# Kernel optimization log

Measured on AMD Instinct MI355X. Metric: run time of the kernel, lower is better.

## Reference

```python
import jax, jax.numpy as jnp
import numpy as np

H = 1024   # longformer-large hidden size
D = 256    # transformer d_model / args.hidden_dim
Q = 100    # num_queries / num_slots
N = 1024   # document length (unpadded tokens)
L = 30     # args.max_span_length
WD = 20    # span width embedding dim
S = N * L - L * (L - 1) // 2  # 30285 candidate spans


def _ln(x, g, b, eps=1e-5):
    m = jnp.mean(x, -1, keepdims=True)
    v = jnp.mean((x - m) ** 2, -1, keepdims=True)
    return (x - m) * jax.lax.rsqrt(v + eps) * g + b


def setup_inputs():
    ks = jax.random.split(jax.random.key(0), 16)
    # deterministic span enumeration: triu(0) & tril(L-1) mention mask, row-major
    idx = np.arange(N)
    m = (idx[None, :] >= idx[:, None]) & (idx[None, :] < idx[:, None] + L)
    ss, ee = np.nonzero(m)
    assert ss.shape[0] == S
    r = lambda i, shape, s=0.02: jax.random.normal(ks[i], shape, jnp.float32) * s
    z = lambda *shape: jnp.zeros(shape, jnp.float32)
    o = lambda *shape: jnp.ones(shape, jnp.float32)
    return dict(
        encoded_doc=jax.random.normal(ks[0], (1, N, H), jnp.float32),
        span_starts=jnp.asarray(ss, jnp.int32),
        span_ends=jnp.asarray(ee, jnp.int32),
        w_word_attn=r(1, (H, 1)), b_word_attn=z(1),
        span_width_embed=r(2, (L, WD)),
        w_span_proj=r(3, (3 * H + WD, D)), b_span_proj=z(D),
        slots_query=r(4, (Q, D)),
        wq=r(5, (D, D)), bq=z(D),
        wk=r(6, (D, D)), bk=z(D),
        wv=r(7, (D, D)), bv=z(D),
        w_ih=r(8, (3 * D, D)), w_hh=r(9, (3 * D, D)), b_ih=z(3 * D), b_hh=z(3 * D),
        w_mlp1=r(10, (D, 2 * D)), b_mlp1=z(2 * D),
        w_mlp2=r(11, (2 * D, D)), b_mlp2=z(D),
        g_in=o(D), beta_in=z(D),
        g_sl=o(D), beta_sl=z(D),
        g_ff=o(D), beta_ff=z(D),
    )


def reference(encoded_doc, span_starts, span_ends, w_word_attn, b_word_attn,
              span_width_embed, w_span_proj, b_span_proj, slots_query,
              wq, bq, wk, bk, wv, bv, w_ih, w_hh, b_ih, b_hh,
              w_mlp1, b_mlp1, w_mlp2, b_mlp2,
              g_in, beta_in, g_sl, beta_sl, g_ff, beta_ff):
    doc = encoded_doc[0]                                   # [N, H]
    # --- get_span_emb ---
    start_emb = doc[span_starts]                           # [S, H]
    end_emb = doc[span_ends]                               # [S, H]
    width_idx = jnp.minimum(1 + span_ends - span_starts, L) - 1
    width_emb = span_width_embed[width_idx]                # [S, WD]
    word_attn = (doc @ w_word_attn)[:, 0] + b_word_attn[0] # [N]
    pos = jnp.arange(N)
    smask = (pos[None, :] >= span_starts[:, None]) & (pos[None, :] <= span_ends[:, None])
    scores = jnp.where(smask, word_attn[None, :], -jnp.inf)  # log(mask)+attn
    head = jax.nn.softmax(scores, axis=-1) @ doc           # [S, H]
    span_emb = jnp.concatenate([start_emb, end_emb, width_emb, head], -1)[None]  # [1,S,3H+WD]
    x = span_emb @ w_span_proj + b_span_proj               # [1, S, D]
    # --- slot attention ---
    inputs = _ln(x, g_in, beta_in)
    k = inputs @ wk + bk
    v = inputs @ wv + bv
    scale = D ** -0.5
    eps = 1e-8
    slots = slots_query[None]                              # [1, Q, D]
    for _ in range(3):
        slots_prev = slots
        q = _ln(slots, g_sl, beta_sl) @ wq + bq
        dots = jnp.einsum('bid,bjd->bij', q, k) * scale    # [1, Q, S]
        attn = jax.nn.softmax(dots, axis=1) + eps          # softmax over slots!
        attn = attn / jnp.sum(attn, -1, keepdims=True)
        updates = jnp.einsum('bjd,bij->bid', v, attn)      # [1, Q, D]
        # torch GRUCell
        xg = updates.reshape(-1, D)
        h = slots_prev.reshape(-1, D)
        gi = xg @ w_ih.T + b_ih
        gh = h @ w_hh.T + b_hh
        ir, iz, inn = jnp.split(gi, 3, -1)
        hr, hz, hn = jnp.split(gh, 3, -1)
        rg = jax.nn.sigmoid(ir + hr)
        zg = jax.nn.sigmoid(iz + hz)
        ng = jnp.tanh(inn + rg * hn)
        slots = ((1.0 - zg) * ng + zg * h).reshape(1, -1, D)
        ff = _ln(slots, g_ff, beta_ff)
        slots = slots + jax.nn.relu(ff @ w_mlp1 + b_mlp1) @ w_mlp2 + b_mlp2
    q = _ln(slots, g_sl, beta_sl) @ wq + bq
    dots = jnp.einsum('bid,bjd->bij', q, k) * scale
    coref_logits = jnp.minimum(jax.nn.softmax(dots, axis=1) + eps, 1.0)  # [1, Q, S]
    return coref_logits, inputs
```

## Files before the change

kernel.cpp:

```cpp
#include <hip/hip_runtime.h>

#define S_TOT 30285
#define SPAD  30720
#define EPS_S 3.0285e-4f

typedef __attribute__((ext_vector_type(8))) short bf16x8;
typedef __attribute__((ext_vector_type(4))) float f32x4;

__device__ __forceinline__ unsigned short f2bf(float f) {
  unsigned u = __float_as_uint(f);
  u += 0x7FFFu + ((u >> 16) & 1u);
  return (unsigned short)(u >> 16);
}
__device__ __forceinline__ float allred_sum(float v) {
#pragma unroll
  for (int o = 32; o > 0; o >>= 1) v += __shfl_xor(v, o, 64);
  return v;
}


__global__ void k_word_attn(const float* __restrict__ doc, const float* __restrict__ w,
                            const float* __restrict__ b, float* __restrict__ wa) {
  int n = blockIdx.x, t = threadIdx.x;
  float s = 0.f;
  for (int h = t; h < 1024; h += 256) s += doc[n * 1024 + h] * w[h];
  __shared__ float red[256];
  red[t] = s;
  __syncthreads();
  for (int o = 128; o; o >>= 1) {
    if (t < o) red[t] += red[t + o];
    __syncthreads();
  }
  if (t == 0) wa[n] = red[0] + b[0];
}

__global__ void k_wd(const float* __restrict__ wemb, const float* __restrict__ wp,
                     float* __restrict__ wd) {
  int w = blockIdx.x, d = threadIdx.x;
  float s = 0.f;
  for (int j = 0; j < 20; j++) s += wemb[w * 20 + j] * wp[(2048 + j) * 256 + d];
  wd[w * 256 + d] = s;
}

__global__ void k_cast3(const float* __restrict__ doc, const float* __restrict__ wih,
                        const float* __restrict__ whh, unsigned short* __restrict__ docb,
                        unsigned short* __restrict__ wihb, unsigned short* __restrict__ whhb) {
  int b = blockIdx.x, t = threadIdx.x;
  if (b < 4096) {
    int i = b * 256 + t;
    docb[i] = f2bf(doc[i]);
  } else if (b < 4864) {
    int i = (b - 4096) * 256 + t;
    wihb[i] = f2bf(wih[i]);
  } else {
    int i = (b - 4864) * 256 + t;
    whhb[i] = f2bf(whh[i]);
  }
}

__global__ void k_tcast_all(const float* __restrict__ wsp, const float* __restrict__ wk,
                            const float* __restrict__ wv, const float* __restrict__ wq,
                            const float* __restrict__ w1, const float* __restrict__ w2,
                            unsigned short* __restrict__ wspT, unsigned short* __restrict__ wkT,
                            unsigned short* __restrict__ wvT, unsigned short* __restrict__ wqT,
                            unsigned short* __restrict__ w1T, unsigned short* __restrict__ w2T) {
  int b = blockIdx.x, t = threadIdx.x;
  const float* src;
  unsigned short* dst;
  int R, C, tid;
  if (b < 768) {
    int sec = b >> 8;
    tid = b & 255;
    src = wsp + (sec == 0 ? 0 : (sec == 1 ? 1024 * 256 : 2068 * 256));
    dst = wspT + (size_t)sec * 256 * 1024;
    R = 1024; C = 256;
  } else if (b < 832) { src = wk; dst = wkT; R = 256; C = 256; tid = b - 768; }
  else if (b < 896) { src = wv; dst = wvT; R = 256; C = 256; tid = b - 832; }
  else if (b < 960) { src = wq; dst = wqT; R = 256; C = 256; tid = b - 896; }
  else if (b < 1088) { src = w1; dst = w1T; R = 256; C = 512; tid = b - 960; }
  else { src = w2; dst = w2T; R = 512; C = 256; tid = b - 1088; }
  int cw = C >> 5;
  int c0 = (tid % cw) * 32, r0 = (tid / cw) * 32;
  __shared__ float tile[32][33];
#pragma unroll
  for (int i = 0; i < 4; i++) {
    int e = i * 256 + t, rr = e >> 5, cc = e & 31;
    tile[rr][cc] = src[(size_t)(r0 + rr) * C + c0 + cc];
  }
  __syncthreads();
#pragma unroll
  for (int i = 0; i < 4; i++) {
    int e = i * 256 + t, cc = e >> 5, rr = e & 31;
    dst[(size_t)(c0 + cc) * R + r0 + rr] = f2bf(tile[rr][cc]);
  }
}

__global__ __launch_bounds__(256) void k_abc_mfma(const unsigned short* __restrict__ docb,
                                                  const unsigned short* __restrict__ wspT,
                                                  float* __restrict__ A, float* __restrict__ B,
                                                  float* __restrict__ C) {
  int rt = blockIdx.x, sec = blockIdx.y;
  float* out = sec == 0 ? A : (sec == 1 ? B : C);
  const unsigned short* wt = wspT + (size_t)sec * 256 * 1024;
  __shared__ unsigned short lds[64 * 256];
  int t = threadIdx.x, w = t >> 6, l = t & 63, lr = l & 15, lh = l >> 4;
  f32x4 acc[4][4];
#pragma unroll
  for (int m = 0; m < 4; m++)
#pragma unroll
    for (int n = 0; n < 4; n++) acc[m][n] = (f32x4){0.f, 0.f, 0.f, 0.f};
  for (int kt = 0; kt < 4; kt++) {
    __syncthreads();
#pragma unroll
    for (int it = 0; it < 8; it++) {
      int e = it * 256 + t, row = e >> 5, c16 = e & 31;
      int ba = ((row * 512) + c16 * 16) ^ ((row & 7) << 4);
      *(uint4*)((char*)lds + ba) =
          *(const uint4*)(docb + (size_t)(rt * 64 + row) * 1024 + kt * 256 + c16 * 8);
    }
    __syncthreads();
    for (int kk = 0; kk < 8; kk++) {
      bf16x8 afr[4];
#pragma unroll
      for (int m = 0; m < 4; m++) {
        int row = m * 16 + lr;
        int ba = ((row * 512) + kk * 64 + lh * 16) ^ ((row & 7) << 4);
        afr[m] = *(bf16x8*)((char*)lds + ba);
      }
#pragma unroll
      for (int n = 0; n < 4; n++) {
        bf16x8 b8 = *(const bf16x8*)(wt + (size_t)(w * 64 + n * 16 + lr) * 1024 + kt * 256 +
                                     kk * 32 + lh * 8);
#pragma unroll
        for (int m = 0; m < 4; m++)
          acc[m][n] = __builtin_amdgcn_mfma_f32_16x16x32_bf16(afr[m], b8, acc[m][n], 0, 0, 0);
      }
    }
  }
#pragma unroll
  for (int n = 0; n < 4; n++) {
    int col = w * 64 + n * 16 + lr;
#pragma unroll
    for (int m = 0; m < 4; m++)
#pragma unroll
      for (int r = 0; r < 4; r++)
        out[(size_t)(rt * 64 + m * 16 + lh * 4 + r) * 256 + col] = acc[m][n][r];
  }
}

__global__ void k_spans_ln(const float* __restrict__ wa, const float* __restrict__ A,
                           const float* __restrict__ B, const float* __restrict__ C,
                           const float* __restrict__ Wd, const float* __restrict__ bias,
                           const float* __restrict__ g_in, const float* __restrict__ be_in,
                           float* __restrict__ xin, unsigned short* __restrict__ inb) {
  int ss = blockIdx.x, t = threadIdx.x;
  int wave = t >> 6, lane = t & 63;
  int nsp = min(30, 1024 - ss);
  int base = (ss < 995) ? ss * 30 : 29850 + 435 - ((1024 - ss) * (1025 - ss)) / 2;
  __shared__ float C_l[30 * 256];
  __shared__ float wa_l[30];
  __shared__ float red[8];
  for (int e = t; e < nsp * 256; e += 256)
    C_l[e] = C[(ss + (e >> 8)) * 256 + (e & 255)];
  if (t < nsp) wa_l[t] = wa[ss + t];
  __syncthreads();
  float aS = A[ss * 256 + t] + bias[t];
  float gg = g_in[t], bb = be_in[t];
  float m = -3.4e38f, Z = 0.f, W = 0.f;
  for (int sp = 0; sp < nsp; sp++) {
    float as_ = wa_l[sp];
    float mn = fmaxf(m, as_);
    float corr = __expf(m - mn);
    float e = __expf(as_ - mn);
    Z = Z * corr + e;
    W = W * corr + e * C_l[sp * 256 + t];
    m = mn;
    float val = aS + B[(ss + sp) * 256 + t] + Wd[sp * 256 + t] + W / Z;
    float s = allred_sum(val);
    if (lane == 0) red[wave] = s;
    __syncthreads();
    float mean = (red[0] + red[1] + red[2] + red[3]) * (1.f / 256.f);
    float dv = val - mean;
    float s2 = allred_sum(dv * dv);
    if (lane == 0) red[4 + wave] = s2;
    __syncthreads();
    float var = (red[4] + red[5] + red[6] + red[7]) * (1.f / 256.f);
    float o = dv * rsqrtf(var + 1e-5f) * gg + bb;
    size_t r = (size_t)(base + sp) * 256 + t;
    xin[r] = o;
    inb[r] = f2bf(o);
    __syncthreads();
  }
}

__global__ __launch_bounds__(256) void k_kv_mfma(const unsigned short* __restrict__ inb,
                                                 const unsigned short* __restrict__ wkT,
                                                 const unsigned short* __restrict__ wvT,
                                                 const float* __restrict__ bk,
                                                 const float* __restrict__ bv,
                                                 unsigned short* __restrict__ kb,
                                                 unsigned short* __restrict__ vT,
                                                 float* __restrict__ vsum) {
  int j0 = blockIdx.x * 64;
  int t = threadIdx.x, w = t >> 6, l = t & 63, lr = l & 15, lh = l >> 4;
  __shared__ unsigned short lds[64 * 256];
#pragma unroll
  for (int it = 0; it < 8; it++) {
    int e = it * 256 + t, row = e >> 5, c16 = e & 31;
    int ba = ((row * 512) + c16 * 16) ^ ((row & 7) << 4);
    *(uint4*)((char*)lds + ba) = *(const uint4*)(inb + (size_t)(j0 + row) * 256 + c16 * 8);
  }
  __syncthreads();
  f32x4 ak[4][4], av[4][4];
#pragma unroll
  for (int m = 0; m < 4; m++)
#pragma unroll
    for (int n = 0; n < 4; n++) {
      ak[m][n] = (f32x4){0.f, 0.f, 0.f, 0.f};
      av[m][n] = (f32x4){0.f, 0.f, 0.f, 0.f};
    }
  for (int kk = 0; kk < 8; kk++) {
    bf16x8 afr[4];
#pragma unroll
    for (int m = 0; m < 4; m++) {
      int row = m * 16 + lr;
      int ba = ((row * 512) + kk * 64 + lh * 16) ^ ((row & 7) << 4);
      afr[m] = *(bf16x8*)((char*)lds + ba);
    }
#pragma unroll
    for (int n = 0; n < 4; n++) {
      int col = w * 64 + n * 16 + lr;
      bf16x8 bk8 = *(const bf16x8*)(wkT + (size_t)col * 256 + kk * 32 + lh * 8);
      bf16x8 bv8 = *(const bf16x8*)(wvT + (size_t)col * 256 + kk * 32 + lh * 8);
#pragma unroll
      for (int m = 0; m < 4; m++) {
        ak[m][n] = __builtin_amdgcn_mfma_f32_16x16x32_bf16(afr[m], bk8, ak[m][n], 0, 0, 0);
        av[m][n] = __builtin_amdgcn_mfma_f32_16x16x32_bf16(afr[m], bv8, av[m][n], 0, 0, 0);
      }
    }
  }
#pragma unroll
  for (int n = 0; n < 4; n++) {
    int col = w * 64 + n * 16 + lr;
    float bks = bk[col], bvs = bv[col];
    float cs = 0.f;
#pragma unroll
    for (int m = 0; m < 4; m++)
#pragma unroll
      for (int r = 0; r < 4; r++) {
        int row = j0 + m * 16 + lh * 4 + r;
        float kvv = ak[m][n][r] + bks;
        float vvv = av[m][n][r] + bvs;
        kb[(size_t)row * 256 + col] = f2bf(kvv);
        vT[(size_t)col * SPAD + row] = f2bf(vvv);
        if (row < S_TOT) cs += vvv;
      }
    cs += __shfl_xor(cs, 16, 64);
    cs += __shfl_xor(cs, 32, 64);
    if (lh == 0) atomicAdd(&vsum[col], cs);
  }
}

__global__ void k_lnq(const float* __restrict__ src, float* __restrict__ slots_w,
                      unsigned short* __restrict__ lnslb, unsigned short* __restrict__ hbf,
                      const float* __restrict__ g, const float* __restrict__ be, int do_copy) {
  int i = blockIdx.x, t = threadIdx.x;
  if (i >= 100) {
    lnslb[i * 256 + t] = 0;
    hbf[i * 256 + t] = 0;
    return;
  }
  int wave = t >> 6, lane = t & 63;
  __shared__ float red[8];
  float v = src[i * 256 + t];
  if (do_copy) slots_w[i * 256 + t] = v;
  hbf[i * 256 + t] = f2bf(v);
  float s = allred_sum(v);
  if (lane == 0) red[wave] = s;
  __syncthreads();
  float mean = (red[0] + red[1] + red[2] + red[3]) * (1.f / 256.f);
  float dv = v - mean;
  float s2 = allred_sum(dv * dv);
  if (lane == 0) red[4 + wave] = s2;
  __syncthreads();
  float var = (red[4] + red[5] + red[6] + red[7]) * (1.f / 256.f);
  float rstd = rsqrtf(var + 1e-5f);
  lnslb[i * 256 + t] = f2bf(dv * rstd * g[t] + be[t]);
}

__global__ __launch_bounds__(256) void k_qmm(const unsigned short* __restrict__ lnslb,
                                             const unsigned short* __restrict__ wqT,
                                             const float* __restrict__ bq,
                                             unsigned short* __restrict__ qbf,
                                             float* __restrict__ rowsum) {
  int t = threadIdx.x;
  if (blockIdx.x == 0 && t < 128) rowsum[t] = 0.f;
  int w = t >> 6, l = t & 63, lr = l & 15, lh = l >> 4;
  int col = blockIdx.x * 64 + w * 16 + lr;
  f32x4 acc[7];
#pragma unroll
  for (int m = 0; m < 7; m++) acc[m] = (f32x4){0.f, 0.f, 0.f, 0.f};
  for (int kk = 0; kk < 8; kk++) {
    int d0 = kk * 32 + lh * 8;
    bf16x8 b8 = *(const bf16x8*)(wqT + (size_t)col * 256 + d0);
#pragma unroll
    for (int m = 0; m < 7; m++) {
      bf16x8 a8 = *(const bf16x8*)(lnslb + (size_t)(m * 16 + lr) * 256 + d0);
      acc[m] = __builtin_amdgcn_mfma_f32_16x16x32_bf16(a8, b8, acc[m], 0, 0, 0);
    }
  }
  float bb = bq[col];
#pragma unroll
  for (int m = 0; m < 7; m++)
#pragma unroll
    for (int r = 0; r < 4; r++)
      qbf[(size_t)(m * 16 + lh * 4 + r) * 256 + col] = f2bf(acc[m][r] + bb);
}

__global__ __launch_bounds__(256) void k_dots_f(const unsigned short* __restrict__ kb,
                                                const unsigned short* __restrict__ qb,
                                                unsigned short* __restrict__ pT,
                                                float* __restrict__ rowsum,
                                                float* __restrict__ uraw,
                                                float* __restrict__ coref, int final_, int S_) {
  int j0 = blockIdx.x * 64;
  int t = threadIdx.x, w = t >> 6, l = t & 63, lr = l & 15, lh = l >> 4;
  if (!final_ && blockIdx.x == 0) {
    for (int e = t; e < 112 * 256; e += 256) uraw[e] = 0.f;
  }
  f32x4 acc[7];
#pragma unroll
  for (int n = 0; n < 7; n++) acc[n] = (f32x4){0.f, 0.f, 0.f, 0.f};
  const unsigned short* arow = kb + (size_t)(j0 + w * 16 + lr) * 256;
  for (int kk = 0; kk < 8; kk++) {
    bf16x8 a8 = *(const bf16x8*)(arow + kk * 32 + lh * 8);
#pragma unroll
    for (int n = 0; n < 7; n++) {
      bf16x8 b8 = *(const bf16x8*)(qb + (size_t)(n * 16 + lr) * 256 + kk * 32 + lh * 8);
      acc[n] = __builtin_amdgcn_mfma_f32_16x16x32_bf16(a8, b8, acc[n], 0, 0, 0);
    }
  }
  __shared__ float dt[64][117];
#pragma unroll
  for (int n = 0; n < 7; n++)
#pragma unroll
    for (int r = 0; r < 4; r++) dt[w * 16 + lh * 4 + r][n * 16 + lr] = acc[n][r] * 0.0625f;
  __syncthreads();
  int jj = t >> 2, q4 = t & 3;
  float mx = -3.4e38f;
#pragma unroll
  for (int i = 0; i < 25; i++) mx = fmaxf(mx, dt[jj][q4 * 25 + i]);
  mx = fmaxf(mx, __shfl_xor(mx, 1, 64));
  mx = fmaxf(mx, __shfl_xor(mx, 2, 64));
  float sm = 0.f;
#pragma unroll
  for (int i = 0; i < 25; i++) {
    float e = __expf(dt[jj][q4 * 25 + i] - mx);
    dt[jj][q4 * 25 + i] = e;
    sm += e;
  }
  sm += __shfl_xor(sm, 1, 64);
  sm += __shfl_xor(sm, 2, 64);
  float inv = 1.f / sm;
#pragma unroll
  for (int i = 0; i < 25; i++) dt[jj][q4 * 25 + i] *= inv;
  __syncthreads();
  if (!final_) {
    for (int e = t; e < 112 * 64; e += 256) {
      int i = e >> 6, j2 = e & 63;
      float pv = (i < 100 && (j0 + j2) < S_) ? dt[j2][i] : 0.f;
      pT[(size_t)i * SPAD + j0 + j2] = f2bf(pv);
    }
    int nv = S_ - j0;
    if (nv > 64) nv = 64;
    if (t < 100) {
      float s = 0.f;
      for (int j2 = 0; j2 < nv; j2++) s += dt[j2][t];
      atomicAdd(rowsum + t, s);
    }
  } else {
    for (int e = t; e < 100 * 64; e += 256) {
      int i = e >> 6, j2 = e & 63;
      if ((j0 + j2) < S_) coref[(size_t)i * S_ + j0 + j2] = fminf(dt[j2][i] + 1e-8f, 1.0f);
    }
  }
}

__global__ __launch_bounds__(256) void k_upd_mfma(const unsigned short* __restrict__ pT,
                                                  const unsigned short* __restrict__ vT,
                                                  float* __restrict__ uraw) {
  int kc = blockIdx.x, ny = blockIdx.y;
  int t = threadIdx.x, w = t >> 6, l = t & 63, lr = l & 15, lh = l >> 4;
  int k0 = kc * 320;
  int c0 = ny * 128 + w * 32;
  f32x4 acc[7][2];
#pragma unroll
  for (int m = 0; m < 7; m++) {
    acc[m][0] = (f32x4){0.f, 0.f, 0.f, 0.f};
    acc[m][1] = (f32x4){0.f, 0.f, 0.f, 0.f};
  }
  for (int ks = 0; ks < 10; ks++) {
    int kof = k0 + ks * 32 + lh * 8;
    bf16x8 b0 = *(const bf16x8*)(vT + (size_t)(c0 + lr) * SPAD + kof);
    bf16x8 b1 = *(const bf16x8*)(vT + (size_t)(c0 + 16 + lr) * SPAD + kof);
#pragma unroll
    for (int m = 0; m < 7; m++) {
      bf16x8 a8 = *(const bf16x8*)(pT + (size_t)(m * 16 + lr) * SPAD + kof);
      acc[m][0] = __builtin_amdgcn_mfma_f32_16x16x32_bf16(a8, b0, acc[m][0], 0, 0, 0);
      acc[m][1] = __builtin_amdgcn_mfma_f32_16x16x32_bf16(a8, b1, acc[m][1], 0, 0, 0);
    }
  }
#pragma unroll
  for (int m = 0; m < 7; m++)
#pragma unroll
    for (int n = 0; n < 2; n++)
#pragma unroll
      for (int r = 0; r < 4; r++) {
        int i = m * 16 + lh * 4 + r;
        if (i < 100) atomicAdd(&uraw[i * 256 + c0 + n * 16 + lr], acc[m][n][r]);
      }
}

__global__ __launch_bounds__(256) void k_gates(
    const float* __restrict__ uraw, const float* __restrict__ vsum,
    const float* __restrict__ rs, const unsigned short* __restrict__ hbf,
    const unsigned short* __restrict__ wihb, const unsigned short* __restrict__ whhb,
    const float* __restrict__ b_ih, const float* __restrict__ b_hh,
    float* __restrict__ gi, float* __restrict__ gh) {
  int x = blockIdx.x, y = blockIdx.y;
  const unsigned short* Wt = y ? whhb : wihb;
  const float* bias = y ? b_hh : b_ih;
  float* out = y ? gh : gi;
  int t = threadIdx.x, w = t >> 6, l = t & 63, lr = l & 15, lh = l >> 4;
  int c0 = x * 128 + w * 32;
  f32x4 acc[7][2];
#pragma unroll
  for (int m = 0; m < 7; m++) {
    acc[m][0] = (f32x4){0.f, 0.f, 0.f, 0.f};
    acc[m][1] = (f32x4){0.f, 0.f, 0.f, 0.f};
  }
  for (int kk = 0; kk < 8; kk++) {
    int d0 = kk * 32 + lh * 8;
    bf16x8 a8[7];
    if (y) {
#pragma unroll
      for (int m = 0; m < 7; m++)
        a8[m] = *(const bf16x8*)(hbf + (size_t)(m * 16 + lr) * 256 + d0);
    } else {
      float4 vs0 = *(const float4*)(vsum + d0);
      float4 vs1 = *(const float4*)(vsum + d0 + 4);
#pragma unroll
      for (int m = 0; m < 7; m++) {
        int row = m * 16 + lr;
        float inv = 1.f / (rs[row] + EPS_S);
        float4 u0 = *(const float4*)(uraw + row * 256 + d0);
        float4 u1 = *(const float4*)(uraw + row * 256 + d0 + 4);
        bf16x8 a;
        a[0] = (short)f2bf((u0.x + 1e-8f * vs0.x) * inv);
        a[1] = (short)f2bf((u0.y + 1e-8f * vs0.y) * inv);
        a[2] = (short)f2bf((u0.z + 1e-8f * vs0.z) * inv);
        a[3] = (short)f2bf((u0.w + 1e-8f * vs0.w) * inv);
        a[4] = (short)f2bf((u1.x + 1e-8f * vs1.x) * inv);
        a[5] = (short)f2bf((u1.y + 1e-8f * vs1.y) * inv);
        a[6] = (short)f2bf((u1.z + 1e-8f * vs1.z) * inv);
        a[7] = (short)f2bf((u1.w + 1e-8f * vs1.w) * inv);
        a8[m] = a;
      }
    }
#pragma unroll
    for (int n = 0; n < 2; n++) {
      bf16x8 b8 = *(const bf16x8*)(Wt + (size_t)(c0 + n * 16 + lr) * 256 + d0);
#pragma unroll
      for (int m = 0; m < 7; m++)
        acc[m][n] = __builtin_amdgcn_mfma_f32_16x16x32_bf16(a8[m], b8, acc[m][n], 0, 0, 0);
    }
  }
#pragma unroll
  for (int n = 0; n < 2; n++) {
    int col = c0 + n * 16 + lr;
    float bb = bias[col];
#pragma unroll
    for (int m = 0; m < 7; m++)
#pragma unroll
      for (int r = 0; r < 4; r++)
        out[(size_t)(m * 16 + lh * 4 + r) * 768 + col] = acc[m][n][r] + bb;
  }
}

__global__ void k_gru2a(const float* __restrict__ gi, const float* __restrict__ gh,
                        const float* __restrict__ slots, float* __restrict__ nsb,
                        unsigned short* __restrict__ ffb, const float* __restrict__ g_ff,
                        const float* __restrict__ be_ff) {
  int i = blockIdx.x, t = threadIdx.x;
  if (i >= 100) {
    ffb[i * 256 + t] = 0;
    return;
  }
  int wave = t >> 6, lane = t & 63;
  __shared__ float red[8];
  float gi0 = gi[i * 768 + t], gi1 = gi[i * 768 + 256 + t], gi2 = gi[i * 768 + 512 + t];
  float gh0 = gh[i * 768 + t], gh1 = gh[i * 768 + 256 + t], gh2 = gh[i * 768 + 512 + t];
  float h = slots[i * 256 + t];
  float rg = 1.f / (1.f + __expf(-(gi0 + gh0)));
  float zg = 1.f / (1.f + __expf(-(gi1 + gh1)));
  float ng = tanhf(gi2 + rg * gh2);
  float ns_ = (1.f - zg) * ng + zg * h;
  nsb[i * 256 + t] = ns_;
  float s = allred_sum(ns_);
  if (lane == 0) red[wave] = s;
  __syncthreads();
  float mean = (red[0] + red[1] + red[2] + red[3]) * (1.f / 256.f);
  float dv = ns_ - mean;
  float s2 = allred_sum(dv * dv);
  if (lane == 0) red[4 + wave] = s2;
  __syncthreads();
  float var = (red[4] + red[5] + red[6] + red[7]) * (1.f / 256.f);
  float o = dv * rsqrtf(var + 1e-5f) * g_ff[t] + be_ff[t];
  ffb[i * 256 + t] = f2bf(o);
}

__global__ __launch_bounds__(256) void k_mlp1(const unsigned short* __restrict__ ffb,
                                              const unsigned short* __restrict__ w1T,
                                              const float* __restrict__ b1,
                                              unsigned short* __restrict__ hidb) {
  int t = threadIdx.x, w = t >> 6, l = t & 63, lr = l & 15, lh = l >> 4;
  int col = blockIdx.x * 64 + w * 16 + lr;
  f32x4 acc[7];
#pragma unroll
  for (int m = 0; m < 7; m++) acc[m] = (f32x4){0.f, 0.f, 0.f, 0.f};
  for (int kk = 0; kk < 8; kk++) {
    int d0 = kk * 32 + lh * 8;
    bf16x8 b8 = *(const bf16x8*)(w1T + (size_t)col * 256 + d0);
#pragma unroll
    for (int m = 0; m < 7; m++) {
      bf16x8 a8 = *(const bf16x8*)(ffb + (size_t)(m * 16 + lr) * 256 + d0);
      acc[m] = __builtin_amdgcn_mfma_f32_16x16x32_bf16(a8, b8, acc[m], 0, 0, 0);
    }
  }
  float bb = b1[col];
#pragma unroll
  for (int m = 0; m < 7; m++)
#pragma unroll
    for (int r = 0; r < 4; r++)
      hidb[(size_t)(m * 16 + lh * 4 + r) * 512 + col] = f2bf(fmaxf(acc[m][r] + bb, 0.f));
}

__global__ __launch_bounds__(256) void k_mlp2(const unsigned short* __restrict__ hidb,
                                              const unsigned short* __restrict__ w2T,
                                              const float* __restrict__ b2,
                                              const float* __restrict__ nsb,
                                              float* __restrict__ slots) {
  int t = threadIdx.x, w = t >> 6, l = t & 63, lr = l & 15, lh = l >> 4;
  int col = blockIdx.x * 64 + w * 16 + lr;
  f32x4 acc[7];
#pragma unroll
  for (int m = 0; m < 7; m++) acc[m] = (f32x4){0.f, 0.f, 0.f, 0.f};
  for (int kk = 0; kk < 16; kk++) {
    int d0 = kk * 32 + lh * 8;
    bf16x8 b8 = *(const bf16x8*)(w2T + (size_t)col * 512 + d0);
#pragma unroll
    for (int m = 0; m < 7; m++) {
      bf16x8 a8 = *(const bf16x8*)(hidb + (size_t)(m * 16 + lr) * 512 + d0);
      acc[m] = __builtin_amdgcn_mfma_f32_16x16x32_bf16(a8, b8, acc[m], 0, 0, 0);
    }
  }
  float bb = b2[col];
#pragma unroll
  for (int m = 0; m < 7; m++)
#pragma unroll
    for (int r = 0; r < 4; r++) {
      int i = m * 16 + lh * 4 + r;
      if (i < 100) slots[i * 256 + col] = acc[m][r] + bb + nsb[i * 256 + col];
    }
}

extern "C" void kernel_launch(void* const* d_in, const int* in_sizes, int n_in,
                              void* d_out, int out_size, void* d_ws, size_t ws_size,
                              hipStream_t stream) {
  const float* doc = (const float*)d_in[0];
  const float* w_wa = (const float*)d_in[3];
  const float* b_wa = (const float*)d_in[4];
  const float* wemb = (const float*)d_in[5];
  const float* wsp = (const float*)d_in[6];
  const float* bsp = (const float*)d_in[7];
  const float* slots_q = (const float*)d_in[8];
  const float* wq = (const float*)d_in[9];
  const float* bq = (const float*)d_in[10];
  const float* wk = (const float*)d_in[11];
  const float* bk = (const float*)d_in[12];
  const float* wv = (const float*)d_in[13];
  const float* bv = (const float*)d_in[14];
  const float* w_ih = (const float*)d_in[15];
  const float* w_hh = (const float*)d_in[16];
  const float* b_ih = (const float*)d_in[17];
  const float* b_hh = (const float*)d_in[18];
  const float* w1 = (const float*)d_in[19];
  const float* b1 = (const float*)d_in[20];
  const float* w2 = (const float*)d_in[21];
  const float* b2 = (const float*)d_in[22];
  const float* g_in = (const float*)d_in[23];
  const float* be_in = (const float*)d_in[24];
  const float* g_sl = (const float*)d_in[25];
  const float* be_sl = (const float*)d_in[26];
  const float* g_ff = (const float*)d_in[27];
  const float* be_ff = (const float*)d_in[28];

  const int S = S_TOT;
  float* out = (float*)d_out;
  float* coref = out;
  float* xin = out + 100 * S;

  float* ws = (float*)d_ws;
  float* wa = ws;
  float* Wd = wa + 1024;
  float* A = Wd + 7680;
  float* Bm = A + 262144;
  float* Cm = Bm + 262144;
  float* vsum = Cm + 262144;
  float* rowsum = vsum + 256;
  float* uraw = rowsum + 128;
  float* slots = uraw + 28672;
  float* nsb = slots + 25600;
  float* gi = nsb + 28672;
  float* gh = gi + 86016;
  unsigned short* ub = (unsigned short*)(gh + 86016);
  unsigned short* inb = ub;
  unsigned short* kbuf = inb + (size_t)SPAD * 256;
  unsigned short* vT = kbuf + (size_t)SPAD * 256;
  unsigned short* pT = vT + (size_t)SPAD * 256;
  unsigned short* qbf = pT + (size_t)112 * SPAD;
  unsigned short* docb = qbf + 112 * 256;
  unsigned short* wspT = docb + 1024 * 1024;
  unsigned short* wkT = wspT + 768 * 1024;
  unsigned short* wvT = wkT + 256 * 256;
  unsigned short* wqT = wvT + 256 * 256;
  unsigned short* wihb = wqT + 256 * 256;
  unsigned short* whhb = wihb + 768 * 256;
  unsigned short* w1T = whhb + 768 * 256;
  unsigned short* w2T = w1T + 512 * 256;
  unsigned short* hbf = w2T + 256 * 512;
  unsigned short* lnslb = hbf + 112 * 256;
  unsigned short* ffb = lnslb + 112 * 256;
  unsigned short* hidb = ffb + 112 * 256;

  k_word_attn<<<1024, 256, 0, stream>>>(doc, w_wa, b_wa, wa);
  k_wd<<<30, 256, 0, stream>>>(wemb, wsp, Wd);
  k_cast3<<<5632, 256, 0, stream>>>(doc, w_ih, w_hh, docb, wihb, whhb);
  k_tcast_all<<<1216, 256, 0, stream>>>(wsp, wk, wv, wq, w1, w2, wspT, wkT, wvT, wqT, w1T, w2T);
  hipMemsetAsync(vsum, 0, 384 * 4, stream);
  hipMemsetAsync(inb + (size_t)S * 256, 0, (size_t)(SPAD - S) * 256 * 2, stream);
  k_abc_mfma<<<dim3(16, 3), 256, 0, stream>>>(docb, wspT, A, Bm, Cm);
  k_spans_ln<<<1024, 256, 0, stream>>>(wa, A, Bm, Cm, Wd, bsp, g_in, be_in, xin, inb);
  k_kv_mfma<<<SPAD / 64, 256, 0, stream>>>(inb, wkT, wvT, bk, bv, kbuf, vT, vsum);
  k_lnq<<<112, 256, 0, stream>>>(slots_q, slots, lnslb, hbf, g_sl, be_sl, 1);

  for (int it = 0; it < 3; ++it) {
    k_qmm<<<4, 256, 0, stream>>>(lnslb, wqT, bq, qbf, rowsum);
    k_dots_f<<<SPAD / 64, 256, 0, stream>>>(kbuf, qbf, pT, rowsum, uraw, coref, 0, S);
    k_upd_mfma<<<dim3(96, 2), 256, 0, stream>>>(pT, vT, uraw);
    k_gates<<<dim3(6, 2), 256, 0, stream>>>(uraw, vsum, rowsum, hbf, wihb, whhb, b_ih, b_hh,
                                            gi, gh);
    k_gru2a<<<112, 256, 0, stream>>>(gi, gh, slots, nsb, ffb, g_ff, be_ff);
    k_mlp1<<<8, 256, 0, stream>>>(ffb, w1T, b1, hidb);
    k_mlp2<<<4, 256, 0, stream>>>(hidb, w2T, b2, nsb, slots);
    k_lnq<<<112, 256, 0, stream>>>(slots, slots, lnslb, hbf, g_sl, be_sl, 0);
  }
  k_qmm<<<4, 256, 0, stream>>>(lnslb, wqT, bq, qbf, rowsum);
  k_dots_f<<<SPAD / 64, 256, 0, stream>>>(kbuf, qbf, pT, rowsum, uraw, coref, 1, S);
}
```

Baseline: 488.4 us.

## Fuse prep kernels, fold layernorms into matmuls, wave-per-span LN in spans kernel

Merges the word-attention, width-embedding, casts, transposes and memsets into one prep kernel. Layer norms are folded into the Q projection and MLP1 prologues, the GRU elementwise step is fused with MLP1, and the gates kernel converts fp32 slots to bf16 itself. The spans kernel now handles one span per wave with float4 lanes and no block barriers. Each iteration gets its own pre-zeroed rowsum/uraw buffers so nothing is cleared in the loop. This cuts launch count and syncs; in exchange every block redundantly recomputes the LN statistics, and k_grumlp1 runs on only 2 blocks.

```diff
diff --git a/kernel.cpp b/kernel.cpp
--- a/kernel.cpp
+++ b/kernel.cpp
@@ -18,80 +18,79 @@
   return v;
 }
 
-
-__global__ void k_word_attn(const float* __restrict__ doc, const float* __restrict__ w,
-                            const float* __restrict__ b, float* __restrict__ wa) {
-  int n = blockIdx.x, t = threadIdx.x;
-  float s = 0.f;
-  for (int h = t; h < 1024; h += 256) s += doc[n * 1024 + h] * w[h];
-  __shared__ float red[256];
-  red[t] = s;
-  __syncthreads();
-  for (int o = 128; o; o >>= 1) {
-    if (t < o) red[t] += red[t + o];
+__global__ void k_prep(const float* __restrict__ doc, const float* __restrict__ w_wa,
+                       const float* __restrict__ b_wa, const float* __restrict__ wemb,
+                       const float* __restrict__ wsp, const float* __restrict__ wk,
+                       const float* __restrict__ wv, const float* __restrict__ wq,
+                       const float* __restrict__ w1, const float* __restrict__ w2,
+                       const float* __restrict__ wih, const float* __restrict__ whh,
+                       const float* __restrict__ slots_q, float* __restrict__ wa,
+                       float* __restrict__ Wd, unsigned short* __restrict__ docb,
+                       unsigned short* __restrict__ wihb, unsigned short* __restrict__ whhb,
+                       unsigned short* __restrict__ wspT, unsigned short* __restrict__ wkT,
+                       unsigned short* __restrict__ wvT, unsigned short* __restrict__ wqT,
+                       unsigned short* __restrict__ w1T, unsigned short* __restrict__ w2T,
+                       float* __restrict__ slots, float* __restrict__ zeroF,
+                       unsigned short* __restrict__ inbpad) {
+  __shared__ float shf[1056];
+  int b = blockIdx.x, t = threadIdx.x;
+  if (b < 1024) {
+    float s = 0.f;
+    for (int h = t; h < 1024; h += 256) s += doc[b * 1024 + h] * w_wa[h];
+    shf[t] = s;
     __syncthreads();
-  }
-  if (t == 0) wa[n] = red[0] + b[0];
-}
-
-__global__ void k_wd(const float* __restrict__ wemb, const float* __restrict__ wp,
-                     float* __restrict__ wd) {
-  int w = blockIdx.x, d = threadIdx.x;
-  float s = 0.f;
-  for (int j = 0; j < 20; j++) s += wemb[w * 20 + j] * wp[(2048 + j) * 256 + d];
-  wd[w * 256 + d] = s;
-}
-
-__global__ void k_cast3(const float* __restrict__ doc, const float* __restrict__ wih,
-                        const float* __restrict__ whh, unsigned short* __restrict__ docb,
-                        unsigned short* __restrict__ wihb, unsigned short* __restrict__ whhb) {
-  int b = blockIdx.x, t = threadIdx.x;
-  if (b < 4096) {
-    int i = b * 256 + t;
-    docb[i] = f2bf(doc[i]);
-  } else if (b < 4864) {
-    int i = (b - 4096) * 256 + t;
-    wihb[i] = f2bf(wih[i]);
+    for (int o = 128; o; o >>= 1) {
+      if (t < o) shf[t] += shf[t + o];
+      __syncthreads();
+    }
+    if (t == 0) wa[b] = shf[0] + b_wa[0];
+  } else if (b < 1054) {
+    int w = b - 1024;
+    float s = 0.f;
+    for (int j = 0; j < 20; j++) s += wemb[w * 20 + j] * wsp[(2048 + j) * 256 + t];
+    Wd[w * 256 + t] = s;
+  } else if (b < 6686) {
+    int b2 = b - 1054;
+    if (b2 < 4096) { int i = b2 * 256 + t; docb[i] = f2bf(doc[i]); }
+    else if (b2 < 4864) { int i = (b2 - 4096) * 256 + t; wihb[i] = f2bf(wih[i]); }
+    else { int i = (b2 - 4864) * 256 + t; whhb[i] = f2bf(whh[i]); }
+  } else if (b < 7902) {
+    int bb = b - 6686;
+    const float* src; unsigned short* dst; int R, C, tid;
+    if (bb < 768) {
+      int sec = bb >> 8; tid = bb & 255;
+      src = wsp + (sec == 0 ? 0 : (sec == 1 ? 1024 * 256 : 2068 * 256));
+      dst = wspT + (size_t)sec * 256 * 1024; R = 1024; C = 256;
+    } else if (bb < 832) { src = wk; dst = wkT; R = 256; C = 256; tid = bb - 768; }
+    else if (bb < 896) { src = wv; dst = wvT; R = 256; C = 256; tid = bb - 832; }
+    else if (bb < 960) { src = wq; dst = wqT; R = 256; C = 256; tid = bb - 896; }
+    else if (bb < 1088) { src = w1; dst = w1T; R = 256; C = 512; tid = bb - 960; }
+    else { src = w2; dst = w2T; R = 512; C = 256; tid = bb - 1088; }
+    int cw = C >> 5;
+    int c0 = (tid % cw) * 32, r0 = (tid / cw) * 32;
+#pragma unroll
+    for (int i = 0; i < 4; i++) {
+      int e = i * 256 + t, rr = e >> 5, cc = e & 31;
+      shf[rr * 33 + cc] = src[(size_t)(r0 + rr) * C + c0 + cc];
+    }
+    __syncthreads();
+#pragma unroll
+    for (int i = 0; i < 4; i++) {
+      int e = i * 256 + t, cc = e >> 5, rr = e & 31;
+      dst[(size_t)(c0 + cc) * R + r0 + rr] = f2bf(shf[rr * 33 + cc]);
+    }
+  } else if (b < 7909) {
+    int r0 = (b - 7902) * 16;
+    for (int rr = 0; rr < 16; rr++) {
+      int row = r0 + rr;
+      slots[row * 256 + t] = (row < 100) ? slots_q[row * 256 + t] : 0.f;
+    }
+  } else if (b < 7994) {
+    int i4 = (b - 7909) * 256 + t;
+    if (i4 < 21664) ((float4*)zeroF)[i4] = (float4){0.f, 0.f, 0.f, 0.f};
   } else {
-    int i = (b - 4864) * 256 + t;
-    whhb[i] = f2bf(whh[i]);
-  }
-}
-
-__global__ void k_tcast_all(const float* __restrict__ wsp, const float* __restrict__ wk,
-                            const float* __restrict__ wv, const float* __restrict__ wq,
-                            const float* __restrict__ w1, const float* __restrict__ w2,
-                            unsigned short* __restrict__ wspT, unsigned short* __restrict__ wkT,
-                            unsigned short* __restrict__ wvT, unsigned short* __restrict__ wqT,
-                            unsigned short* __restrict__ w1T, unsigned short* __restrict__ w2T) {
-  int b = blockIdx.x, t = threadIdx.x;
-  const float* src;
-  unsigned short* dst;
-  int R, C, tid;
-  if (b < 768) {
-    int sec = b >> 8;
-    tid = b & 255;
-    src = wsp + (sec == 0 ? 0 : (sec == 1 ? 1024 * 256 : 2068 * 256));
-    dst = wspT + (size_t)sec * 256 * 1024;
-    R = 1024; C = 256;
-  } else if (b < 832) { src = wk; dst = wkT; R = 256; C = 256; tid = b - 768; }
-  else if (b < 896) { src = wv; dst = wvT; R = 256; C = 256; tid = b - 832; }
-  else if (b < 960) { src = wq; dst = wqT; R = 256; C = 256; tid = b - 896; }
-  else if (b < 1088) { src = w1; dst = w1T; R = 256; C = 512; tid = b - 960; }
-  else { src = w2; dst = w2T; R = 512; C = 256; tid = b - 1088; }
-  int cw = C >> 5;
-  int c0 = (tid % cw) * 32, r0 = (tid / cw) * 32;
-  __shared__ float tile[32][33];
-#pragma unroll
-  for (int i = 0; i < 4; i++) {
-    int e = i * 256 + t, rr = e >> 5, cc = e & 31;
-    tile[rr][cc] = src[(size_t)(r0 + rr) * C + c0 + cc];
-  }
-  __syncthreads();
-#pragma unroll
-  for (int i = 0; i < 4; i++) {
-    int e = i * 256 + t, cc = e >> 5, rr = e & 31;
-    dst[(size_t)(c0 + cc) * R + r0 + rr] = f2bf(tile[rr][cc]);
+    int i = (b - 7994) * 256 + t;
+    if (i < 13920) ((uint4*)inbpad)[i] = (uint4){0u, 0u, 0u, 0u};
   }
 }
 
@@ -154,42 +153,59 @@
                            const float* __restrict__ g_in, const float* __restrict__ be_in,
                            float* __restrict__ xin, unsigned short* __restrict__ inb) {
   int ss = blockIdx.x, t = threadIdx.x;
-  int wave = t >> 6, lane = t & 63;
+  int w = t >> 6, lane = t & 63;
   int nsp = min(30, 1024 - ss);
   int base = (ss < 995) ? ss * 30 : 29850 + 435 - ((1024 - ss) * (1025 - ss)) / 2;
   __shared__ float C_l[30 * 256];
   __shared__ float wa_l[30];
-  __shared__ float red[8];
   for (int e = t; e < nsp * 256; e += 256)
     C_l[e] = C[(ss + (e >> 8)) * 256 + (e & 255)];
   if (t < nsp) wa_l[t] = wa[ss + t];
   __syncthreads();
-  float aS = A[ss * 256 + t] + bias[t];
-  float gg = g_in[t], bb = be_in[t];
-  float m = -3.4e38f, Z = 0.f, W = 0.f;
-  for (int sp = 0; sp < nsp; sp++) {
-    float as_ = wa_l[sp];
-    float mn = fmaxf(m, as_);
-    float corr = __expf(m - mn);
-    float e = __expf(as_ - mn);
-    Z = Z * corr + e;
-    W = W * corr + e * C_l[sp * 256 + t];
-    m = mn;
-    float val = aS + B[(ss + sp) * 256 + t] + Wd[sp * 256 + t] + W / Z;
-    float s = allred_sum(val);
-    if (lane == 0) red[wave] = s;
-    __syncthreads();
-    float mean = (red[0] + red[1] + red[2] + red[3]) * (1.f / 256.f);
-    float dv = val - mean;
-    float s2 = allred_sum(dv * dv);
-    if (lane == 0) red[4 + wave] = s2;
-    __syncthreads();
-    float var = (red[4] + red[5] + red[6] + red[7]) * (1.f / 256.f);
-    float o = dv * rsqrtf(var + 1e-5f) * gg + bb;
-    size_t r = (size_t)(base + sp) * 256 + t;
-    xin[r] = o;
-    inb[r] = f2bf(o);
-    __syncthreads();
+  int c0 = lane * 4;
+  float4 aS = *(const float4*)(A + ss * 256 + c0);
+  float4 bi = *(const float4*)(bias + c0);
+  float a0 = aS.x + bi.x, a1 = aS.y + bi.y, a2 = aS.z + bi.z, a3 = aS.w + bi.w;
+  float4 gg = *(const float4*)(g_in + c0);
+  float4 bb = *(const float4*)(be_in + c0);
+  float m = -3.4e38f, Z = 0.f;
+  float W0 = 0.f, W1 = 0.f, W2 = 0.f, W3 = 0.f;
+  int pos = 0;
+  for (int sp = w; sp < nsp; sp += 4) {
+    for (; pos <= sp; ++pos) {
+      float as_ = wa_l[pos];
+      float mn = fmaxf(m, as_);
+      float corr = __expf(m - mn);
+      float e = __expf(as_ - mn);
+      Z = Z * corr + e;
+      float4 cc = *(const float4*)(C_l + pos * 256 + c0);
+      W0 = W0 * corr + e * cc.x;
+      W1 = W1 * corr + e * cc.y;
+      W2 = W2 * corr + e * cc.z;
+      W3 = W3 * corr + e * cc.w;
+      m = mn;
+    }
+    float invZ = 1.f / Z;
+    float4 Bv = *(const float4*)(B + (size_t)(ss + sp) * 256 + c0);
+    float4 wd = *(const float4*)(Wd + sp * 256 + c0);
+    float v0 = a0 + Bv.x + wd.x + W0 * invZ;
+    float v1 = a1 + Bv.y + wd.y + W1 * invZ;
+    float v2 = a2 + Bv.z + wd.z + W2 * invZ;
+    float v3 = a3 + Bv.w + wd.w + W3 * invZ;
+    float s = allred_sum(v0 + v1 + v2 + v3);
+    float mean = s * (1.f / 256.f);
+    float d0 = v0 - mean, d1 = v1 - mean, d2 = v2 - mean, d3 = v3 - mean;
+    float q = allred_sum(d0 * d0 + d1 * d1 + d2 * d2 + d3 * d3);
+    float rstd = rsqrtf(q * (1.f / 256.f) + 1e-5f);
+    float o0 = d0 * rstd * gg.x + bb.x;
+    float o1 = d1 * rstd * gg.y + bb.y;
+    float o2 = d2 * rstd * gg.z + bb.z;
+    float o3 = d3 * rstd * gg.w + bb.w;
+    size_t r = (size_t)(base + sp) * 256 + c0;
+    *(float4*)(xin + r) = (float4){o0, o1, o2, o3};
+    ushort4 u4;
+    u4.x = f2bf(o0); u4.y = f2bf(o1); u4.z = f2bf(o2); u4.w = f2bf(o3);
+    *(ushort4*)(inb + r) = u4;
   }
 }
 
@@ -261,52 +277,52 @@
   }
 }
 
-__global__ void k_lnq(const float* __restrict__ src, float* __restrict__ slots_w,
-                      unsigned short* __restrict__ lnslb, unsigned short* __restrict__ hbf,
-                      const float* __restrict__ g, const float* __restrict__ be, int do_copy) {
-  int i = blockIdx.x, t = threadIdx.x;
-  if (i >= 100) {
-    lnslb[i * 256 + t] = 0;
-    hbf[i * 256 + t] = 0;
-    return;
-  }
-  int wave = t >> 6, lane = t & 63;
-  __shared__ float red[8];
-  float v = src[i * 256 + t];
-  if (do_copy) slots_w[i * 256 + t] = v;
-  hbf[i * 256 + t] = f2bf(v);
-  float s = allred_sum(v);
-  if (lane == 0) red[wave] = s;
+__global__ __launch_bounds__(256) void k_qmmln(const float* __restrict__ slots,
+                                               const float* __restrict__ g,
+                                               const float* __restrict__ be,
+                                               const unsigned short* __restrict__ wqT,
+                                               const float* __restrict__ bq,
+                                               unsigned short* __restrict__ qbf) {
+  __shared__ float stat[112][2];
+  int t = threadIdx.x, w = t >> 6, lane = t & 63;
+  for (int row = w; row < 112; row += 4) {
+    float4 v = *(const float4*)(slots + row * 256 + lane * 4);
+    float s = allred_sum(v.x + v.y + v.z + v.w);
+    float q = allred_sum(v.x * v.x + v.y * v.y + v.z * v.z + v.w * v.w);
+    if (lane == 0) {
+      float mean = s * (1.f / 256.f);
+      float var = fmaxf(q * (1.f / 256.f) - mean * mean, 0.f);
+      stat[row][0] = mean;
+      stat[row][1] = rsqrtf(var + 1e-5f);
+    }
+  }
   __syncthreads();
-  float mean = (red[0] + red[1] + red[2] + red[3]) * (1.f / 256.f);
-  float dv = v - mean;
-  float s2 = allred_sum(dv * dv);
-  if (lane == 0) red[4 + wave] = s2;
-  __syncthreads();
-  float var = (red[4] + red[5] + red[6] + red[7]) * (1.f / 256.f);
-  float rstd = rsqrtf(var + 1e-5f);
-  lnslb[i * 256 + t] = f2bf(dv * rstd * g[t] + be[t]);
-}
-
-__global__ __launch_bounds__(256) void k_qmm(const unsigned short* __restrict__ lnslb,
-                                             const unsigned short* __restrict__ wqT,
-                                             const float* __restrict__ bq,
-                                             unsigned short* __restrict__ qbf,
-                                             float* __restrict__ rowsum) {
-  int t = threadIdx.x;
-  if (blockIdx.x == 0 && t < 128) rowsum[t] = 0.f;
-  int w = t >> 6, l = t & 63, lr = l & 15, lh = l >> 4;
+  int lr = lane & 15, lh = lane >> 4;
   int col = blockIdx.x * 64 + w * 16 + lr;
   f32x4 acc[7];
 #pragma unroll
   for (int m = 0; m < 7; m++) acc[m] = (f32x4){0.f, 0.f, 0.f, 0.f};
   for (int kk = 0; kk < 8; kk++) {
     int d0 = kk * 32 + lh * 8;
+    float4 g0 = *(const float4*)(g + d0), g1 = *(const float4*)(g + d0 + 4);
+    float4 e0 = *(const float4*)(be + d0), e1 = *(const float4*)(be + d0 + 4);
     bf16x8 b8 = *(const bf16x8*)(wqT + (size_t)col * 256 + d0);
 #pragma unroll
     for (int m = 0; m < 7; m++) {
-      bf16x8 a8 = *(const bf16x8*)(lnslb + (size_t)(m * 16 + lr) * 256 + d0);
-      acc[m] = __builtin_amdgcn_mfma_f32_16x16x32_bf16(a8, b8, acc[m], 0, 0, 0);
+      int row = m * 16 + lr;
+      float mean = stat[row][0], rstd = stat[row][1];
+      float4 u0 = *(const float4*)(slots + row * 256 + d0);
+      float4 u1 = *(const float4*)(slots + row * 256 + d0 + 4);
+      bf16x8 a;
+      a[0] = (short)f2bf((u0.x - mean) * rstd * g0.x + e0.x);
+      a[1] = (short)f2bf((u0.y - mean) * rstd * g0.y + e0.y);
+      a[2] = (short)f2bf((u0.z - mean) * rstd * g0.z + e0.z);
+      a[3] = (short)f2bf((u0.w - mean) * rstd * g0.w + e0.w);
+      a[4] = (short)f2bf((u1.x - mean) * rstd * g1.x + e1.x);
+      a[5] = (short)f2bf((u1.y - mean) * rstd * g1.y + e1.y);
+      a[6] = (short)f2bf((u1.z - mean) * rstd * g1.z + e1.z);
+      a[7] = (short)f2bf((u1.w - mean) * rstd * g1.w + e1.w);
+      acc[m] = __builtin_amdgcn_mfma_f32_16x16x32_bf16(a, b8, acc[m], 0, 0, 0);
     }
   }
   float bb = bq[col];
@@ -321,13 +337,9 @@
                                                 const unsigned short* __restrict__ qb,
                                                 unsigned short* __restrict__ pT,
                                                 float* __restrict__ rowsum,
-                                                float* __restrict__ uraw,
                                                 float* __restrict__ coref, int final_, int S_) {
   int j0 = blockIdx.x * 64;
   int t = threadIdx.x, w = t >> 6, l = t & 63, lr = l & 15, lh = l >> 4;
-  if (!final_ && blockIdx.x == 0) {
-    for (int e = t; e < 112 * 256; e += 256) uraw[e] = 0.f;
-  }
   f32x4 acc[7];
 #pragma unroll
   for (int n = 0; n < 7; n++) acc[n] = (f32x4){0.f, 0.f, 0.f, 0.f};
@@ -423,7 +435,7 @@
 
 __global__ __launch_bounds__(256) void k_gates(
     const float* __restrict__ uraw, const float* __restrict__ vsum,
-    const float* __restrict__ rs, const unsigned short* __restrict__ hbf,
+    const float* __restrict__ rs, const float* __restrict__ slots,
     const unsigned short* __restrict__ wihb, const unsigned short* __restrict__ whhb,
     const float* __restrict__ b_ih, const float* __restrict__ b_hh,
     float* __restrict__ gi, float* __restrict__ gh) {
@@ -444,8 +456,17 @@
     bf16x8 a8[7];
     if (y) {
 #pragma unroll
-      for (int m = 0; m < 7; m++)
-        a8[m] = *(const bf16x8*)(hbf + (size_t)(m * 16 + lr) * 256 + d0);
+      for (int m = 0; m < 7; m++) {
+        int row = m * 16 + lr;
+        float4 h0 = *(const float4*)(slots + row * 256 + d0);
+        float4 h1 = *(const float4*)(slots + row * 256 + d0 + 4);
+        bf16x8 a;
+        a[0] = (short)f2bf(h0.x); a[1] = (short)f2bf(h0.y);
+        a[2] = (short)f2bf(h0.z); a[3] = (short)f2bf(h0.w);
+        a[4] = (short)f2bf(h1.x); a[5] = (short)f2bf(h1.y);
+        a[6] = (short)f2bf(h1.z); a[7] = (short)f2bf(h1.w);
+        a8[m] = a;
+      }
     } else {
       float4 vs0 = *(const float4*)(vsum + d0);
       float4 vs1 = *(const float4*)(vsum + d0 + 4);
@@ -487,62 +508,84 @@
   }
 }
 
-__global__ void k_gru2a(const float* __restrict__ gi, const float* __restrict__ gh,
-                        const float* __restrict__ slots, float* __restrict__ nsb,
-                        unsigned short* __restrict__ ffb, const float* __restrict__ g_ff,
-                        const float* __restrict__ be_ff) {
-  int i = blockIdx.x, t = threadIdx.x;
-  if (i >= 100) {
-    ffb[i * 256 + t] = 0;
-    return;
-  }
-  int wave = t >> 6, lane = t & 63;
-  __shared__ float red[8];
-  float gi0 = gi[i * 768 + t], gi1 = gi[i * 768 + 256 + t], gi2 = gi[i * 768 + 512 + t];
-  float gh0 = gh[i * 768 + t], gh1 = gh[i * 768 + 256 + t], gh2 = gh[i * 768 + 512 + t];
-  float h = slots[i * 256 + t];
-  float rg = 1.f / (1.f + __expf(-(gi0 + gh0)));
-  float zg = 1.f / (1.f + __expf(-(gi1 + gh1)));
-  float ng = tanhf(gi2 + rg * gh2);
-  float ns_ = (1.f - zg) * ng + zg * h;
-  nsb[i * 256 + t] = ns_;
-  float s = allred_sum(ns_);
-  if (lane == 0) red[wave] = s;
+__global__ __launch_bounds__(256) void k_grumlp1(
+    const float* __restrict__ gi, const float* __restrict__ gh,
+    const float* __restrict__ slots, float* __restrict__ nsb,
+    const float* __restrict__ g_ff, const float* __restrict__ be_ff,
+    const unsigned short* __restrict__ w1T, const float* __restrict__ b1,
+    unsigned short* __restrict__ hidb) {
+  __shared__ float stat[112][2];
+  int t = threadIdx.x, w = t >> 6, lane = t & 63;
+  for (int e = t; e < 112 * 256; e += 256) {
+    int i = e >> 8, c = e & 255;
+    float gi0 = gi[i * 768 + c], gi1 = gi[i * 768 + 256 + c], gi2 = gi[i * 768 + 512 + c];
+    float gh0 = gh[i * 768 + c], gh1 = gh[i * 768 + 256 + c], gh2 = gh[i * 768 + 512 + c];
+    float h = slots[e];
+    float rg = 1.f / (1.f + __expf(-(gi0 + gh0)));
+    float zg = 1.f / (1.f + __expf(-(gi1 + gh1)));
+    float ng = tanhf(gi2 + rg * gh2);
+    nsb[e] = (1.f - zg) * ng + zg * h;
+  }
   __syncthreads();
-  float mean = (red[0] + red[1] + red[2] + red[3]) * (1.f / 256.f);
-  float dv = ns_ - mean;
-  float s2 = allred_sum(dv * dv);
-  if (lane == 0) red[4 + wave] = s2;
+  for (int row = w; row < 112; row += 4) {
+    float4 v = *(const float4*)(nsb + row * 256 + lane * 4);
+    float s = allred_sum(v.x + v.y + v.z + v.w);
+    float q = allred_sum(v.x * v.x + v.y * v.y + v.z * v.z + v.w * v.w);
+    if (lane == 0) {
+      float mean = s * (1.f / 256.f);
+      float var = fmaxf(q * (1.f / 256.f) - mean * mean, 0.f);
+      stat[row][0] = mean;
+      stat[row][1] = rsqrtf(var + 1e-5f);
+    }
+  }
   __syncthreads();
-  float var = (red[4] + red[5] + red[6] + red[7]) * (1.f / 256.f);
-  float o = dv * rsqrtf(var + 1e-5f) * g_ff[t] + be_ff[t];
-  ffb[i * 256 + t] = f2bf(o);
-}
-
-__global__ __launch_bounds__(256) void k_mlp1(const unsigned short* __restrict__ ffb,
-                                              const unsigned short* __restrict__ w1T,
-                                              const float* __restrict__ b1,
-                                              unsigned short* __restrict__ hidb) {
-  int t = threadIdx.x, w = t >> 6, l = t & 63, lr = l & 15, lh = l >> 4;
-  int col = blockIdx.x * 64 + w * 16 + lr;
-  f32x4 acc[7];
-#pragma unroll
-  for (int m = 0; m < 7; m++) acc[m] = (f32x4){0.f, 0.f, 0.f, 0.f};
+  int lr = lane & 15, lh = lane >> 4;
+  f32x4 acc[7][4];
+#pragma unroll
+  for (int m = 0; m < 7; m++)
+#pragma unroll
+    for (int n = 0; n < 4; n++) acc[m][n] = (f32x4){0.f, 0.f, 0.f, 0.f};
   for (int kk = 0; kk < 8; kk++) {
     int d0 = kk * 32 + lh * 8;
-    bf16x8 b8 = *(const bf16x8*)(w1T + (size_t)col * 256 + d0);
+    float4 g0 = *(const float4*)(g_ff + d0), g1 = *(const float4*)(g_ff + d0 + 4);
+    float4 e0 = *(const float4*)(be_ff + d0), e1 = *(const float4*)(be_ff + d0 + 4);
+    bf16x8 a8[7];
 #pragma unroll
     for (int m = 0; m < 7; m++) {
-      bf16x8 a8 = *(const bf16x8*)(ffb + (size_t)(m * 16 + lr) * 256 + d0);
-      acc[m] = __builtin_amdgcn_mfma_f32_16x16x32_bf16(a8, b8, acc[m], 0, 0, 0);
-    }
-  }
-  float bb = b1[col];
-#pragma unroll
-  for (int m = 0; m < 7; m++)
-#pragma unroll
-    for (int r = 0; r < 4; r++)
-      hidb[(size_t)(m * 16 + lh * 4 + r) * 512 + col] = f2bf(fmaxf(acc[m][r] + bb, 0.f));
+      int row = m * 16 + lr;
+      float mean = stat[row][0], rstd = stat[row][1];
+      float4 u0 = *(const float4*)(nsb + row * 256 + d0);
+      float4 u1 = *(const float4*)(nsb + row * 256 + d0 + 4);
+      bf16x8 a;
+      a[0] = (short)f2bf((u0.x - mean) * rstd * g0.x + e0.x);
+      a[1] = (short)f2bf((u0.y - mean) * rstd * g0.y + e0.y);
+      a[2] = (short)f2bf((u0.z - mean) * rstd * g0.z + e0.z);
+      a[3] = (short)f2bf((u0.w - mean) * rstd * g0.w + e0.w);
+      a[4] = (short)f2bf((u1.x - mean) * rstd * g1.x + e1.x);
+      a[5] = (short)f2bf((u1.y - mean) * rstd * g1.y + e1.y);
+      a[6] = (short)f2bf((u1.z - mean) * rstd * g1.z + e1.z);
+      a[7] = (short)f2bf((u1.w - mean) * rstd * g1.w + e1.w);
+      a8[m] = a;
+    }
+#pragma unroll
+    for (int n = 0; n < 4; n++) {
+      int col = blockIdx.x * 256 + w * 64 + n * 16 + lr;
+      bf16x8 b8 = *(const bf16x8*)(w1T + (size_t)col * 256 + d0);
+#pragma unroll
+      for (int m = 0; m < 7; m++)
+        acc[m][n] = __builtin_amdgcn_mfma_f32_16x16x32_bf16(a8[m], b8, acc[m][n], 0, 0, 0);
+    }
+  }
+#pragma unroll
+  for (int n = 0; n < 4; n++) {
+    int col = blockIdx.x * 256 + w * 64 + n * 16 + lr;
+    float bb = b1[col];
+#pragma unroll
+    for (int m = 0; m < 7; m++)
+#pragma unroll
+      for (int r = 0; r < 4; r++)
+        hidb[(size_t)(m * 16 + lh * 4 + r) * 512 + col] = f2bf(fmaxf(acc[m][n][r] + bb, 0.f));
+  }
 }
 
 __global__ __launch_bounds__(256) void k_mlp2(const unsigned short* __restrict__ hidb,
@@ -618,9 +661,9 @@
   float* Cm = Bm + 262144;
   float* vsum = Cm + 262144;
   float* rowsum = vsum + 256;
-  float* uraw = rowsum + 128;
-  float* slots = uraw + 28672;
-  float* nsb = slots + 25600;
+  float* uraw = rowsum + 384;
+  float* slots = uraw + 86016;
+  float* nsb = slots + 28672;
   float* gi = nsb + 28672;
   float* gh = gi + 86016;
   unsigned short* ub = (unsigned short*)(gh + 86016);
@@ -638,33 +681,27 @@
   unsigned short* whhb = wihb + 768 * 256;
   unsigned short* w1T = whhb + 768 * 256;
   unsigned short* w2T = w1T + 512 * 256;
-  unsigned short* hbf = w2T + 256 * 512;
-  unsigned short* lnslb = hbf + 112 * 256;
-  unsigned short* ffb = lnslb + 112 * 256;
-  unsigned short* hidb = ffb + 112 * 256;
-
-  k_word_attn<<<1024, 256, 0, stream>>>(doc, w_wa, b_wa, wa);
-  k_wd<<<30, 256, 0, stream>>>(wemb, wsp, Wd);
-  k_cast3<<<5632, 256, 0, stream>>>(doc, w_ih, w_hh, docb, wihb, whhb);
-  k_tcast_all<<<1216, 256, 0, stream>>>(wsp, wk, wv, wq, w1, w2, wspT, wkT, wvT, wqT, w1T, w2T);
-  hipMemsetAsync(vsum, 0, 384 * 4, stream);
-  hipMemsetAsync(inb + (size_t)S * 256, 0, (size_t)(SPAD - S) * 256 * 2, stream);
+  unsigned short* hidb = w2T + 256 * 512;
+
+  k_prep<<<8049, 256, 0, stream>>>(doc, w_wa, b_wa, wemb, wsp, wk, wv, wq, w1, w2,
+                                   w_ih, w_hh, slots_q, wa, Wd, docb, wihb, whhb, wspT,
+                                   wkT, wvT, wqT, w1T, w2T, slots, vsum,
+                                   inb + (size_t)S * 256);
   k_abc_mfma<<<dim3(16, 3), 256, 0, stream>>>(docb, wspT, A, Bm, Cm);
   k_spans_ln<<<1024, 256, 0, stream>>>(wa, A, Bm, Cm, Wd, bsp, g_in, be_in, xin, inb);
   k_kv_mfma<<<SPAD / 64, 256, 0, stream>>>(inb, wkT, wvT, bk, bv, kbuf, vT, vsum);
-  k_lnq<<<112, 256, 0, stream>>>(slots_q, slots, lnslb, hbf, g_sl, be_sl, 1);
 
   for (int it = 0; it < 3; ++it) {
-    k_qmm<<<4, 256, 0, stream>>>(lnslb, wqT, bq, qbf, rowsum);
-    k_dots_f<<<SPAD / 64, 256, 0, stream>>>(kbuf, qbf, pT, rowsum, uraw, coref, 0, S);
-    k_upd_mfma<<<dim3(96, 2), 256, 0, stream>>>(pT, vT, uraw);
-    k_gates<<<dim3(6, 2), 256, 0, stream>>>(uraw, vsum, rowsum, hbf, wihb, whhb, b_ih, b_hh,
-                                            gi, gh);
-    k_gru2a<<<112, 256, 0, stream>>>(gi, gh, slots, nsb, ffb, g_ff, be_ff);
-    k_mlp1<<<8, 256, 0, stream>>>(ffb, w1T, b1, hidb);
+    float* rs_it = rowsum + it * 128;
+    float* uraw_it = uraw + it * 28672;
+    k_qmmln<<<4, 256, 0, stream>>>(slots, g_sl, be_sl, wqT, bq, qbf);
+    k_dots_f<<<SPAD / 64, 256, 0, stream>>>(kbuf, qbf, pT, rs_it, coref, 0, S);
+    k_upd_mfma<<<dim3(96, 2), 256, 0, stream>>>(pT, vT, uraw_it);
+    k_gates<<<dim3(6, 2), 256, 0, stream>>>(uraw_it, vsum, rs_it, slots, wihb, whhb,
+                                            b_ih, b_hh, gi, gh);
+    k_grumlp1<<<2, 256, 0, stream>>>(gi, gh, slots, nsb, g_ff, be_ff, w1T, b1, hidb);
     k_mlp2<<<4, 256, 0, stream>>>(hidb, w2T, b2, nsb, slots);
-    k_lnq<<<112, 256, 0, stream>>>(slots, slots, lnslb, hbf, g_sl, be_sl, 0);
-  }
-  k_qmm<<<4, 256, 0, stream>>>(lnslb, wqT, bq, qbf, rowsum);
-  k_dots_f<<<SPAD / 64, 256, 0, stream>>>(kbuf, qbf, pT, rowsum, uraw, coref, 1, S);
-}
+  }
+  k_qmmln<<<4, 256, 0, stream>>>(slots, g_sl, be_sl, wqT, bq, qbf);
+  k_dots_f<<<SPAD / 64, 256, 0, stream>>>(kbuf, qbf, pT, rowsum, coref, 1, S);
+}
```

Measured after the change: 789.8 us. 61.7% more time.
